# Optimization experiments

Hardware: AMD Instinct MI355X
Metric: run time of the kernel (lower is better)

## Reference

```python
import jax, jax.numpy as jnp
import numpy as np

B, D, H, W = 32, 256, 32, 32
K = 1024
BETA = 0.25


def setup_inputs() -> dict:
    key = jax.random.key(0)
    k1, k2 = jax.random.split(key)
    z_e = jax.random.normal(k1, (B, D, H, W), dtype=jnp.float32)
    codebook_weight = jax.random.normal(k2, (K, D), dtype=jnp.float32)
    return {"z_e": z_e, "codebook_weight": codebook_weight}


def reference(z_e, codebook_weight):
    # NCHW -> NHWC, flatten to tokens [N, D]
    z_perm = jnp.transpose(z_e, (0, 2, 3, 1))            # [B, H, W, D]
    z_flat = z_perm.reshape(-1, codebook_weight.shape[1])  # [N, D]

    # Squared Euclidean distances (argmin-equivalent to torch.cdist argmin)
    # d2[n, k] = ||z_n||^2 - 2 z_n . c_k + ||c_k||^2
    d2 = (jnp.sum(z_flat * z_flat, axis=1, keepdims=True)
          - 2.0 * (z_flat @ codebook_weight.T)
          + jnp.sum(codebook_weight * codebook_weight, axis=1)[None, :])  # [N, K]
    codebook_idx = jnp.argmin(d2, axis=1)                 # [N]

    # one-hot @ codebook == gather
    z_quant = codebook_weight[codebook_idx].reshape(z_perm.shape)  # [B,H,W,D]

    # straight-through estimator, back to NCHW
    z_q = z_perm + jax.lax.stop_gradient(z_quant - z_perm)
    z_q = jnp.transpose(z_q, (0, 3, 1, 2))                # [B, D, H, W]

    loss_codebook = jnp.mean((z_quant - jax.lax.stop_gradient(z_perm)) ** 2)
    loss_commit = jnp.mean((jax.lax.stop_gradient(z_quant) - z_perm) ** 2)
    loss_vq = loss_codebook + loss_commit * BETA

    return z_q, codebook_idx[:, None], loss_vq
```

## Files before the change

kernel.cpp:

```cpp
#include <hip/hip_runtime.h>
#include <hip/hip_bf16.h>
#include <cstdint>

#define B_ 32
#define D_ 256
#define K_ 1024
#define N_TOK 32768
#define Z_ELEMS 8388608
#define OUT_IDX_OFF Z_ELEMS
#define OUT_LOSS_OFF (Z_ELEMS + N_TOK)

#define WS_CNORM_OFF 0
#define WS_PART_OFF  4096
#define WS_CBF_OFF   8192
#define WS_TOP2_OFF  532480

#define MARGIN 1.25f

typedef __attribute__((ext_vector_type(8))) short short8v;
typedef __attribute__((ext_vector_type(4))) float f32x4;
typedef unsigned long long u64;

__device__ __forceinline__ unsigned short f2bf(float x) {
    unsigned u = __float_as_uint(x);
    return (unsigned short)((u + 0x7fffu + ((u >> 16) & 1u)) >> 16);
}
__device__ __forceinline__ unsigned packf(float f) {
    unsigned u = __float_as_uint(f);
    return (u & 0x80000000u) ? ~u : (u | 0x80000000u);
}
__device__ __forceinline__ float unpackf(unsigned p) {
    unsigned u = (p & 0x80000000u) ? (p & 0x7fffffffu) : ~p;
    return __uint_as_float(u);
}

__global__ __launch_bounds__(256)
void prep_kernel(const float* __restrict__ cb, float* __restrict__ cnorm,
                 unsigned char* __restrict__ cbf) {
    const int t = threadIdx.x;
    const int blk = blockIdx.x;
    {
        int k = blk * 64 + (t >> 2);
        int part = t & 3;
        const float4* row = reinterpret_cast<const float4*>(cb + k * D_);
        float s = 0.f;
#pragma unroll
        for (int j = 0; j < 16; ++j) {
            float4 v = row[part * 16 + j];
            s += v.x * v.x + v.y * v.y + v.z * v.z + v.w * v.w;
        }
        s += __shfl_xor(s, 1);
        s += __shfl_xor(s, 2);
        if (part == 0) cnorm[k] = s;
    }
#pragma unroll
    for (int w = 0; w < 8; ++w) {
        int g = blk * 2048 + w * 256 + t;
        int lane = g & 63, ct = (g >> 6) & 7, kc = (g >> 9) & 7, cblk = g >> 12;
        int code = cblk * 128 + ct * 16 + (lane & 15);
        int d0 = kc * 32 + (lane >> 4) * 8;
        const float* src = cb + code * 256 + d0;
        float4 a = *reinterpret_cast<const float4*>(src);
        float4 b2 = *reinterpret_cast<const float4*>(src + 4);
        uint4 pk;
        pk.x = (unsigned)f2bf(a.x) | ((unsigned)f2bf(a.y) << 16);
        pk.y = (unsigned)f2bf(a.z) | ((unsigned)f2bf(a.w) << 16);
        pk.z = (unsigned)f2bf(b2.x) | ((unsigned)f2bf(b2.y) << 16);
        pk.w = (unsigned)f2bf(b2.z) | ((unsigned)f2bf(b2.w) << 16);
        *reinterpret_cast<uint4*>(cbf + (size_t)g * 16) = pk;
    }
}

__global__ __launch_bounds__(256, 2)
void screen_kernel(const float* __restrict__ z, const unsigned char* __restrict__ cbf,
                   const float* __restrict__ cnorm, unsigned* __restrict__ top2) {
    __shared__ __align__(16) unsigned char zfB[32768];
    __shared__ float cns[1024];

    const int t = threadIdx.x;
    const int lane = t & 63;
    const int wv = t >> 6;
    const int blk = blockIdx.x;
    const int b = blk >> 4;
    const int hw0 = (blk & 15) << 6;
    const float* zb = z + ((size_t)b << 18) + hw0;

    for (int i = t; i < 1024; i += 256) cns[i] = cnorm[i];

    {
        const int tok = t & 63;
        const int dseg = t >> 6;
#pragma unroll
        for (int u = 0; u < 8; ++u) {
            int d0 = dseg * 64 + u * 8;
            float v[8];
#pragma unroll
            for (int j = 0; j < 8; ++j) v[j] = zb[(size_t)(d0 + j) * 1024 + tok];
            uint4 pk;
            pk.x = (unsigned)f2bf(v[0]) | ((unsigned)f2bf(v[1]) << 16);
            pk.y = (unsigned)f2bf(v[2]) | ((unsigned)f2bf(v[3]) << 16);
            pk.z = (unsigned)f2bf(v[4]) | ((unsigned)f2bf(v[5]) << 16);
            pk.w = (unsigned)f2bf(v[6]) | ((unsigned)f2bf(v[7]) << 16);
            int kc = d0 >> 5;
            int slot = (kc * 4 + (tok >> 4)) * 64 + (u & 3) * 16 + (tok & 15);
            *reinterpret_cast<uint4*>(zfB + slot * 16) = pk;
        }
    }
    __syncthreads();

    const int rbase = (lane >> 4) << 2;

#pragma unroll
    for (int cb2 = 0; cb2 < 2; ++cb2) {
        const int cblk = wv * 2 + cb2;
        const unsigned char* abase = cbf + (size_t)cblk * 65536 + lane * 16;

        f32x4 acc[8][4];
#pragma unroll
        for (int mt = 0; mt < 8; ++mt)
#pragma unroll
            for (int nt = 0; nt < 4; ++nt) acc[mt][nt] = (f32x4){0.f, 0.f, 0.f, 0.f};

#pragma unroll
        for (int kc = 0; kc < 8; ++kc) {
            short8v bfv[4];
#pragma unroll
            for (int nt = 0; nt < 4; ++nt)
                bfv[nt] = *reinterpret_cast<const short8v*>(zfB + (kc * 4 + nt) * 1024 + lane * 16);
            short8v af[8];
#pragma unroll
            for (int mt = 0; mt < 8; ++mt)
                af[mt] = *reinterpret_cast<const short8v*>(abase + (kc * 8 + mt) * 1024);
#pragma unroll
            for (int mt = 0; mt < 8; ++mt)
#pragma unroll
                for (int nt = 0; nt < 4; ++nt)
                    acc[mt][nt] = __builtin_amdgcn_mfma_f32_16x16x32_bf16(
                        af[mt], bfv[nt], acc[mt][nt], 0, 0, 0);
        }

#pragma unroll
        for (int nt = 0; nt < 4; ++nt) {
            unsigned k1 = 0xFFFFFFFFu, k2 = 0xFFFFFFFFu;
#pragma unroll
            for (int mt = 0; mt < 8; ++mt) {
#pragma unroll
                for (int r = 0; r < 4; ++r) {
                    int code = cblk * 128 + mt * 16 + rbase + r;
                    float d2a = fmaf(-2.0f, acc[mt][nt][r], cns[code]);
                    unsigned key = (packf(d2a) & 0xFFFFFC00u) | (unsigned)code;
                    if (key < k1) { k2 = k1; k1 = key; }
                    else if (key < k2) { k2 = key; }
                }
            }
#pragma unroll
            for (int x = 16; x <= 32; x <<= 1) {
                unsigned o1 = __shfl_xor(k1, x);
                unsigned o2 = __shfl_xor(k2, x);
                unsigned n1, n2;
                if (k1 < o1) { n1 = k1; n2 = (k2 < o1) ? k2 : o1; }
                else         { n1 = o1; n2 = (o2 < k1) ? o2 : k1; }
                k1 = n1; k2 = n2;
            }
            if (lane < 16) {
                int token = blk * 64 + nt * 16 + lane;
                *reinterpret_cast<uint2*>(top2 + ((size_t)cblk * N_TOK + token) * 2) =
                    make_uint2(k1, k2);
            }
        }
    }
}

__global__ __launch_bounds__(256)
void refgather_kernel(const float* __restrict__ z, const float* __restrict__ cb,
                      const float* __restrict__ cnorm, const unsigned* __restrict__ top2,
                      float* __restrict__ out, float* __restrict__ partials) {
    __shared__ float zsm[32][261];
    __shared__ float crows[32][257];
    __shared__ int cand[32][16];
    __shared__ int cnt[32];
    __shared__ u64 bestk[32];
    __shared__ int sidx[32];
    __shared__ float red[256];
    __shared__ int maxc;

    const int t = threadIdx.x;
    const int bh = blockIdx.x;
    const int b = bh >> 5, h = bh & 31;
    const int n0 = b * 1024 + h * 32;
    const int w = t & 31, dg = t >> 5;

    {
        const float* zp = z + ((size_t)b << 18) + h * 32 + w;
#pragma unroll
        for (int i = 0; i < 32; ++i) {
            int d = dg * 32 + i;
            zsm[w][d] = zp[(size_t)d * 1024];
        }
    }
    if (t < 32) cnt[t] = 0;
    if (t == 0) maxc = 0;
    __syncthreads();

    const int tk = t >> 3, l8 = t & 7;
    {
        uint2 kk = *reinterpret_cast<const uint2*>(
            top2 + ((size_t)l8 * N_TOK + (n0 + tk)) * 2);
        unsigned mn = kk.x;
#pragma unroll
        for (int x = 1; x < 8; x <<= 1) {
            unsigned o = __shfl_xor(mn, x);
            if (o < mn) mn = o;
        }
        float thr = unpackf(mn & 0xFFFFFC00u) + MARGIN;
        float da = unpackf(kk.x & 0xFFFFFC00u);
        if (da <= thr) { int p = atomicAdd(&cnt[tk], 1); cand[tk][p] = (int)(kk.x & 1023u); }
        float db = unpackf(kk.y & 0xFFFFFC00u);
        if (db <= thr) { int p = atomicAdd(&cnt[tk], 1); cand[tk][p] = (int)(kk.y & 1023u); }
    }
    __syncthreads();
    if (t < 32) atomicMax(&maxc, cnt[t]);
    __syncthreads();

    const int mc = maxc;
    u64 best = ~0ull;
    for (int ci = 0; ci < mc; ++ci) {
        if (ci < cnt[tk]) {
            int k = cand[tk][ci];
            const float* crow = cb + (size_t)k * 256;
            float s = 0.f;
#pragma unroll
            for (int j = 0; j < 32; ++j) {
                int d = j * 8 + l8;
                s = fmaf(zsm[tk][d], crow[d], s);
            }
#pragma unroll
            for (int x = 1; x < 8; x <<= 1) s += __shfl_xor(s, x);
            float d2 = cnorm[k] - 2.f * s;
            u64 key = ((u64)packf(d2) << 32) | (unsigned)k;
            if (key < best) best = key;
        }
    }
    if (l8 == 0) bestk[tk] = best;
    __syncthreads();
    if (t < 32) {
        int k = (int)(bestk[t] & 1023ull);
        sidx[t] = k;
        out[OUT_IDX_OFF + n0 + t] = (float)k;
    }
    __syncthreads();
    {
        const int r = t & 31, q = t >> 5;
        const float4* src = reinterpret_cast<const float4*>(cb + (size_t)sidx[r] * 256 + q * 32);
#pragma unroll
        for (int j = 0; j < 8; ++j) {
            float4 v = src[j];
            int d = q * 32 + j * 4;
            crows[r][d] = v.x; crows[r][d + 1] = v.y;
            crows[r][d + 2] = v.z; crows[r][d + 3] = v.w;
        }
    }
    __syncthreads();
    float accl = 0.f;
    float* orow = out + ((size_t)b << 18) + h * 32 + w;
#pragma unroll
    for (int i = 0; i < 32; ++i) {
        const int d = dg * 32 + i;
        const float cv = crows[w][d];
        const float zv = zsm[w][d];
        orow[(size_t)d * 1024] = cv;
        const float df = cv - zv;
        accl += df * df;
    }
    red[t] = accl;
    __syncthreads();
    for (int s = 128; s > 0; s >>= 1) {
        if (t < s) red[t] += red[t + s];
        __syncthreads();
    }
    if (t == 0) partials[bh] = red[0];
}

__global__ __launch_bounds__(256) void loss_kernel(const float* __restrict__ partials,
                                                   float* __restrict__ out) {
    __shared__ float red[256];
    const int t = threadIdx.x;
    float s = partials[t] + partials[t + 256] + partials[t + 512] + partials[t + 768];
    red[t] = s;
    __syncthreads();
    for (int st = 128; st > 0; st >>= 1) {
        if (t < st) red[t] += red[t + st];
        __syncthreads();
    }
    if (t == 0) out[OUT_LOSS_OFF] = red[0] * (1.25f / (float)Z_ELEMS);
}

extern "C" void kernel_launch(void* const* d_in, const int* in_sizes, int n_in,
                              void* d_out, int out_size, void* d_ws, size_t ws_size,
                              hipStream_t stream) {
    const float* z = (const float*)d_in[0];
    const float* cb = (const float*)d_in[1];
    float* out = (float*)d_out;
    float* cnorm = (float*)((char*)d_ws + WS_CNORM_OFF);
    float* partials = (float*)((char*)d_ws + WS_PART_OFF);
    unsigned char* cbf = (unsigned char*)d_ws + WS_CBF_OFF;
    unsigned* top2 = (unsigned*)((char*)d_ws + WS_TOP2_OFF);

    prep_kernel<<<16, 256, 0, stream>>>(cb, cnorm, cbf);
    screen_kernel<<<512, 256, 0, stream>>>(z, cbf, cnorm, top2);
    refgather_kernel<<<1024, 256, 0, stream>>>(z, cb, cnorm, top2, out, partials);
    loss_kernel<<<1, 256, 0, stream>>>(partials, out);
}
```

Measured before the change: 70.78 us.

## Split screen kernel across 8 waves, one codebook block each, halving accumulator tiles

The screening kernel now launches 512 threads per block, with each of 8 waves handling one 128-code block instead of 4 waves handling two each. Each wave processes its block in two passes of 64 codes, so it holds 16 accumulator tiles instead of 32, and it keeps a running top-2 per token across the passes. The aim is lower register pressure and more resident waves to hide memory and MFMA latency. In exchange, the z tile in LDS is reread across passes and per-wave work shrinks, which adds relative overhead.

```diff
diff --git a/kernel.cpp b/kernel.cpp
--- a/kernel.cpp
+++ b/kernel.cpp
@@ -71,7 +71,7 @@
     }
 }
 
-__global__ __launch_bounds__(256, 2)
+__global__ __launch_bounds__(512, 4)
 void screen_kernel(const float* __restrict__ z, const unsigned char* __restrict__ cbf,
                    const float* __restrict__ cnorm, unsigned* __restrict__ top2) {
     __shared__ __align__(16) unsigned char zfB[32768];
@@ -85,14 +85,14 @@
     const int hw0 = (blk & 15) << 6;
     const float* zb = z + ((size_t)b << 18) + hw0;
 
-    for (int i = t; i < 1024; i += 256) cns[i] = cnorm[i];
+    for (int i = t; i < 1024; i += 512) cns[i] = cnorm[i];
 
     {
         const int tok = t & 63;
-        const int dseg = t >> 6;
-#pragma unroll
-        for (int u = 0; u < 8; ++u) {
-            int d0 = dseg * 64 + u * 8;
+        const int kc = t >> 6;
+#pragma unroll
+        for (int u = 0; u < 4; ++u) {
+            int d0 = kc * 32 + u * 8;
             float v[8];
 #pragma unroll
             for (int j = 0; j < 8; ++j) v[j] = zb[(size_t)(d0 + j) * 1024 + tok];
@@ -101,23 +101,25 @@
             pk.y = (unsigned)f2bf(v[2]) | ((unsigned)f2bf(v[3]) << 16);
             pk.z = (unsigned)f2bf(v[4]) | ((unsigned)f2bf(v[5]) << 16);
             pk.w = (unsigned)f2bf(v[6]) | ((unsigned)f2bf(v[7]) << 16);
-            int kc = d0 >> 5;
-            int slot = (kc * 4 + (tok >> 4)) * 64 + (u & 3) * 16 + (tok & 15);
+            int slot = (kc * 4 + (tok >> 4)) * 64 + u * 16 + (tok & 15);
             *reinterpret_cast<uint4*>(zfB + slot * 16) = pk;
         }
     }
     __syncthreads();
 
     const int rbase = (lane >> 4) << 2;
-
-#pragma unroll
-    for (int cb2 = 0; cb2 < 2; ++cb2) {
-        const int cblk = wv * 2 + cb2;
-        const unsigned char* abase = cbf + (size_t)cblk * 65536 + lane * 16;
-
-        f32x4 acc[8][4];
-#pragma unroll
-        for (int mt = 0; mt < 8; ++mt)
+    const unsigned char* abase = cbf + (size_t)wv * 65536 + lane * 16;
+    const unsigned char* zrd = zfB + lane * 16;
+
+    unsigned k1[4], k2[4];
+#pragma unroll
+    for (int nt = 0; nt < 4; ++nt) { k1[nt] = 0xFFFFFFFFu; k2[nt] = 0xFFFFFFFFu; }
+
+#pragma unroll
+    for (int p = 0; p < 2; ++p) {
+        f32x4 acc[4][4];
+#pragma unroll
+        for (int mt = 0; mt < 4; ++mt)
 #pragma unroll
             for (int nt = 0; nt < 4; ++nt) acc[mt][nt] = (f32x4){0.f, 0.f, 0.f, 0.f};
 
@@ -126,47 +128,50 @@
             short8v bfv[4];
 #pragma unroll
             for (int nt = 0; nt < 4; ++nt)
-                bfv[nt] = *reinterpret_cast<const short8v*>(zfB + (kc * 4 + nt) * 1024 + lane * 16);
-            short8v af[8];
-#pragma unroll
-            for (int mt = 0; mt < 8; ++mt)
-                af[mt] = *reinterpret_cast<const short8v*>(abase + (kc * 8 + mt) * 1024);
-#pragma unroll
-            for (int mt = 0; mt < 8; ++mt)
+                bfv[nt] = *reinterpret_cast<const short8v*>(zrd + (kc * 4 + nt) * 1024);
+#pragma unroll
+            for (int mt = 0; mt < 4; ++mt) {
+                short8v af = *reinterpret_cast<const short8v*>(
+                    abase + (kc * 8 + p * 4 + mt) * 1024);
 #pragma unroll
                 for (int nt = 0; nt < 4; ++nt)
                     acc[mt][nt] = __builtin_amdgcn_mfma_f32_16x16x32_bf16(
-                        af[mt], bfv[nt], acc[mt][nt], 0, 0, 0);
+                        af, bfv[nt], acc[mt][nt], 0, 0, 0);
+            }
         }
 
 #pragma unroll
         for (int nt = 0; nt < 4; ++nt) {
-            unsigned k1 = 0xFFFFFFFFu, k2 = 0xFFFFFFFFu;
-#pragma unroll
-            for (int mt = 0; mt < 8; ++mt) {
+#pragma unroll
+            for (int mt = 0; mt < 4; ++mt) {
 #pragma unroll
                 for (int r = 0; r < 4; ++r) {
-                    int code = cblk * 128 + mt * 16 + rbase + r;
+                    int code = wv * 128 + (p * 4 + mt) * 16 + rbase + r;
                     float d2a = fmaf(-2.0f, acc[mt][nt][r], cns[code]);
                     unsigned key = (packf(d2a) & 0xFFFFFC00u) | (unsigned)code;
-                    if (key < k1) { k2 = k1; k1 = key; }
-                    else if (key < k2) { k2 = key; }
+                    if (key < k1[nt]) { k2[nt] = k1[nt]; k1[nt] = key; }
+                    else if (key < k2[nt]) { k2[nt] = key; }
                 }
             }
-#pragma unroll
-            for (int x = 16; x <= 32; x <<= 1) {
-                unsigned o1 = __shfl_xor(k1, x);
-                unsigned o2 = __shfl_xor(k2, x);
-                unsigned n1, n2;
-                if (k1 < o1) { n1 = k1; n2 = (k2 < o1) ? k2 : o1; }
-                else         { n1 = o1; n2 = (o2 < k1) ? o2 : k1; }
-                k1 = n1; k2 = n2;
-            }
-            if (lane < 16) {
-                int token = blk * 64 + nt * 16 + lane;
-                *reinterpret_cast<uint2*>(top2 + ((size_t)cblk * N_TOK + token) * 2) =
-                    make_uint2(k1, k2);
-            }
+        }
+    }
+
+#pragma unroll
+    for (int nt = 0; nt < 4; ++nt) {
+        unsigned a1 = k1[nt], a2 = k2[nt];
+#pragma unroll
+        for (int x = 16; x <= 32; x <<= 1) {
+            unsigned o1 = __shfl_xor(a1, x);
+            unsigned o2 = __shfl_xor(a2, x);
+            unsigned n1, n2;
+            if (a1 < o1) { n1 = a1; n2 = (a2 < o1) ? a2 : o1; }
+            else         { n1 = o1; n2 = (o2 < a1) ? o2 : a1; }
+            a1 = n1; a2 = n2;
+        }
+        if (lane < 16) {
+            int token = blk * 64 + nt * 16 + lane;
+            *reinterpret_cast<uint2*>(top2 + ((size_t)wv * N_TOK + token) * 2) =
+                make_uint2(a1, a2);
         }
     }
 }
@@ -307,7 +312,7 @@
     unsigned* top2 = (unsigned*)((char*)d_ws + WS_TOP2_OFF);
 
     prep_kernel<<<16, 256, 0, stream>>>(cb, cnorm, cbf);
-    screen_kernel<<<512, 256, 0, stream>>>(z, cbf, cnorm, top2);
+    screen_kernel<<<512, 512, 0, stream>>>(z, cbf, cnorm, top2);
     refgather_kernel<<<1024, 256, 0, stream>>>(z, cb, cnorm, top2, out, partials);
     loss_kernel<<<1, 256, 0, stream>>>(partials, out);
 }
```

New measurement: 166.0 us. 135% more time.
